# Kernel optimization log

Measured on AMD Instinct MI355X. Metric: run time of the kernel, lower is better.

## Reference

```python
import jax, jax.numpy as jnp
import numpy as np

B = 512      # batch
H = 64       # latent_dim == GRU hidden size
F = 32       # n_features
S = 2048     # seq_len
NEG_SLOPE = 0.01  # nn.LeakyReLU default


def setup_inputs() -> dict:
    key = jax.random.key(0)
    ks = jax.random.split(key, 14)

    def p(k, shape, scale=0.1):
        return jax.random.normal(k, shape, dtype=jnp.float32) * scale

    return {
        "noise": jax.random.normal(ks[0], (B, H), dtype=jnp.float32),
        # GRU forward direction (layer 0): weight_ih_l0, weight_hh_l0, biases
        "W_ih_f": p(ks[1], (3 * H, H)),
        "W_hh_f": p(ks[2], (3 * H, H)),
        "b_ih_f": p(ks[3], (3 * H,)),
        "b_hh_f": p(ks[4], (3 * H,)),
        # GRU backward direction (layer 0 reverse)
        "W_ih_b": p(ks[5], (3 * H, H)),
        "W_hh_b": p(ks[6], (3 * H, H)),
        "b_ih_b": p(ks[7], (3 * H,)),
        "b_hh_b": p(ks[8], (3 * H,)),
        # latent_linear: Linear(2H -> H)
        "W_lat": p(ks[9], (H, 2 * H)),
        "b_lat": p(ks[10], (H,)),
        # output_linear: Linear(H -> F)
        "W_out": p(ks[11], (F, H)),
        "b_out": p(ks[12], (F,)),
    }


def _leaky(x):
    return jnp.where(x >= 0, x, NEG_SLOPE * x)


def _gru_cell(x, h, W_ih, W_hh, b_ih, b_hh):
    # PyTorch GRU cell: gates ordered (r, z, n)
    gi = x @ W_ih.T + b_ih          # (B, 3H)
    gh = h @ W_hh.T + b_hh          # (B, 3H)
    i_r, i_z, i_n = jnp.split(gi, 3, axis=-1)
    h_r, h_z, h_n = jnp.split(gh, 3, axis=-1)
    r = jax.nn.sigmoid(i_r + h_r)
    z = jax.nn.sigmoid(i_z + h_z)
    n = jnp.tanh(i_n + r * h_n)
    return (1.0 - z) * n + z * h


def reference(noise, W_ih_f, W_hh_f, b_ih_f, b_hh_f,
              W_ih_b, W_hh_b, b_ih_b, b_hh_b,
              W_lat, b_lat, W_out, b_out):
    # hidden_state = noise.repeat((D*n_layers,1,1)) -> both directions start at noise
    batch = noise.shape[0]

    def step(carry, _):
        x, hf, hb = carry
        # GRU on a length-1 sequence: each direction does one cell update;
        # output timestep = concat(fwd_out, bwd_out)
        hf2 = _gru_cell(x, hf, W_ih_f, W_hh_f, b_ih_f, b_hh_f)
        hb2 = _gru_cell(x, hb, W_ih_b, W_hh_b, b_ih_b, b_hh_b)
        out = jnp.concatenate([hf2, hb2], axis=-1)        # (B, 2H)
        lat = _leaky(out @ W_lat.T + b_lat)               # (B, H)
        return (lat, hf2, hb2), lat

    x0 = jnp.zeros((batch, H), dtype=noise.dtype)
    _, ys = jax.lax.scan(step, (x0, noise, noise), None, length=S)
    seq = jnp.transpose(ys, (1, 0, 2))   # (B, S, H)
    seq = _leaky(seq)                    # second LeakyReLU as in the original
    out = jax.nn.sigmoid(seq @ W_out.T + b_out)  # (B, S, F)
    return out
```

## Files before the change

kernel.cpp:

```cpp
#include <hip/hip_runtime.h>
#include <hip/hip_bf16.h>


#define NBATCH 512
#define NH 64
#define NS 2048
#define NF 32
#define MROW 16
#define LDH 72

typedef short s16x4 __attribute__((ext_vector_type(4)));
typedef short s16x8 __attribute__((ext_vector_type(8)));
typedef float f32x4 __attribute__((ext_vector_type(4)));

#define MFMA(a, b, c) __builtin_amdgcn_mfma_f32_16x16x32_bf16((a), (b), (c), 0, 0, 0)

#define NLOG2E  (-1.4426950408889634f)
#define N2LOG2E (-2.8853900817779268f)

__device__ __forceinline__ short f2bf(float f) {
    return (short)((__float_as_uint(f) + 0x8000u) >> 16);
}

__device__ __forceinline__ f32x4 v_exp2(f32x4 a) {
    f32x4 r;
#pragma unroll
    for (int i = 0; i < 4; ++i) r[i] = __builtin_amdgcn_exp2f(a[i]);
    return r;
}

__device__ __forceinline__ f32x4 v_rcp(f32x4 a) {
    f32x4 r;
#pragma unroll
    for (int i = 0; i < 4; ++i) r[i] = __builtin_amdgcn_rcpf(a[i]);
    return r;
}

__device__ __forceinline__ f32x4 v_lk(f32x4 a) {
    f32x4 b = a * 0.01f;
    f32x4 r;
#pragma unroll
    for (int i = 0; i < 4; ++i) r[i] = fmaxf(a[i], b[i]);
    return r;
}

__device__ __forceinline__ f32x4 v_sigm(f32x4 a) {
    return v_rcp(v_exp2(a * NLOG2E) + 1.0f);
}

__device__ __forceinline__ int2 pk4bf(f32x4 v) {
    union { __hip_bfloat162 b; int i; } lo, hi;
    float2 a; a.x = v[0]; a.y = v[1];
    float2 b; b.x = v[2]; b.y = v[3];
    lo.b = __float22bfloat162_rn(a);
    hi.b = __float22bfloat162_rn(b);
    int2 r; r.x = lo.i; r.y = hi.i;
    return r;
}

__device__ __forceinline__ s16x8 bfragW(const float* __restrict__ W, int ldk,
                                        int row, int kf, int quad) {
    const float* p = W + (size_t)row * ldk + kf * 32 + quad * 8;
    s16x8 r;
#pragma unroll
    for (int i = 0; i < 8; ++i) r[i] = f2bf(p[i]);
    return r;
}

__device__ __forceinline__ f32x4 bias4(const float* __restrict__ p) {
    const float4 v = *(const float4*)p;
    f32x4 r = {v.x, v.y, v.z, v.w};
    return r;
}

__global__ __launch_bounds__(512)
__attribute__((amdgpu_waves_per_eu(2, 2)))
void grugan_kernel(const float* __restrict__ noise,
                   const float* __restrict__ Wihf, const float* __restrict__ Whhf,
                   const float* __restrict__ bihf, const float* __restrict__ bhhf,
                   const float* __restrict__ Wihb, const float* __restrict__ Whhb,
                   const float* __restrict__ bihb, const float* __restrict__ bhhb,
                   const float* __restrict__ Wlat, const float* __restrict__ blat,
                   const float* __restrict__ Wout, const float* __restrict__ bout,
                   float* __restrict__ out)
{
    __shared__ __align__(16) short Xs[2][MROW][LDH];
    __shared__ __align__(16) short X2s[2][MROW][LDH];
    __shared__ __align__(16) short Hs[2][2][MROW][LDH];

    const int tid  = threadIdx.x;
    const int wave = tid >> 6;
    const int lane = tid & 63;
    const int n    = lane & 15;
    const int quad = lane >> 4;
    const int row0 = blockIdx.x * MROW;

    const int dir  = wave >> 2;
    const int cb   = wave & 3;
    const int jrow = cb * 16 + n;
    const int jq   = cb * 16 + quad * 4;
    const float* Wih = dir ? Wihb : Wihf;
    const float* Whh = dir ? Whhb : Whhf;
    const float* bih = dir ? bihb : bihf;
    const float* bhh = dir ? bhhb : bhhf;

    s16x8 wir0 = bfragW(Wih, NH,   0 + jrow, 0, quad);
    s16x8 wir1 = bfragW(Wih, NH,   0 + jrow, 1, quad);
    s16x8 wiz0 = bfragW(Wih, NH,  64 + jrow, 0, quad);
    s16x8 wiz1 = bfragW(Wih, NH,  64 + jrow, 1, quad);
    s16x8 win0 = bfragW(Wih, NH, 128 + jrow, 0, quad);
    s16x8 win1 = bfragW(Wih, NH, 128 + jrow, 1, quad);
    s16x8 whr0 = bfragW(Whh, NH,   0 + jrow, 0, quad);
    s16x8 whr1 = bfragW(Whh, NH,   0 + jrow, 1, quad);
    s16x8 whz0 = bfragW(Whh, NH,  64 + jrow, 0, quad);
    s16x8 whz1 = bfragW(Whh, NH,  64 + jrow, 1, quad);
    s16x8 whn0 = bfragW(Whh, NH, 128 + jrow, 0, quad);
    s16x8 whn1 = bfragW(Whh, NH, 128 + jrow, 1, quad);
    f32x4 initR, initZ;
    {
        f32x4 a = bias4(&bih[jq]),      b = bias4(&bhh[jq]);
        initR = a + b;
        f32x4 c = bias4(&bih[64 + jq]), d = bias4(&bhh[64 + jq]);
        initZ = c + d;
    }
    const f32x4 initN1 = bias4(&bih[128 + jq]);
    const f32x4 initN2 = bias4(&bhh[128 + jq]);

    const int nq = (wave & 3) * 16 + quad * 4;
    s16x8 wl0 = bfragW(Wlat, 2 * NH, (wave & 3) * 16 + n, 0, quad);
    s16x8 wl1 = bfragW(Wlat, 2 * NH, (wave & 3) * 16 + n, 1, quad);
    s16x8 wl2 = bfragW(Wlat, 2 * NH, (wave & 3) * 16 + n, 2, quad);
    s16x8 wl3 = bfragW(Wlat, 2 * NH, (wave & 3) * 16 + n, 3, quad);
    const f32x4 initL = bias4(&blat[(wave & 3) * 16 + quad * 4]);

    const int f0 = (wave & 1) * 16;
    s16x8 wo0 = bfragW(Wout, NH, f0 + n, 0, quad);
    s16x8 wo1 = bfragW(Wout, NH, f0 + n, 1, quad);
    const f32x4 initO = bias4(&bout[f0 + quad * 4]);
    float* const orow = out + (size_t)(row0 + n) * (NS * NF) + f0 + quad * 4;

    for (int idx = tid; idx < MROW * LDH; idx += 512) (&Xs[0][0][0])[idx] = 0;
    f32x4 hreg;
    {
        const float4 nz = *(const float4*)&noise[(size_t)(row0 + n) * NH + jq];
        hreg[0] = nz.x; hreg[1] = nz.y; hreg[2] = nz.z; hreg[3] = nz.w;
        *(int2*)&Hs[0][dir][n][jq] = pk4bf(hreg);
    }
    __syncthreads();

    f32x4 accR, accZ, accN2;
    {
        s16x8 ha0 = *(const s16x8*)&Hs[0][dir][n][quad * 8];
        s16x8 ha1 = *(const s16x8*)&Hs[0][dir][n][32 + quad * 8];
        accR  = MFMA(whr0, ha0, initR);  accR  = MFMA(whr1, ha1, accR);
        accZ  = MFMA(whz0, ha0, initZ);  accZ  = MFMA(whz1, ha1, accZ);
        accN2 = MFMA(whn0, ha0, initN2); accN2 = MFMA(whn1, ha1, accN2);
    }

    f32x4 yv = {0.f, 0.f, 0.f, 0.f};

#define STEP(HB, T) do {                                                        \
    if ((T) >= 2 && wave >= 6)                                                  \
        *(f32x4*)(orow + (size_t)((T) - 2) * NF) = yv;                          \
    {                                                                           \
        s16x8 xa0 = *(const s16x8*)&Xs[HB][n][quad * 8];                        \
        s16x8 xa1 = *(const s16x8*)&Xs[HB][n][32 + quad * 8];                   \
        accR = MFMA(wir0, xa0, accR);   accR = MFMA(wir1, xa1, accR);           \
        accZ = MFMA(wiz0, xa0, accZ);   accZ = MFMA(wiz1, xa1, accZ);           \
        f32x4 accN1 = MFMA(win0, xa0, initN1);                                  \
        accN1 = MFMA(win1, xa1, accN1);                                         \
         \
         \
         \
        f32x4 eR = v_exp2(accR * NLOG2E);                                       \
        f32x4 rr = v_rcp(eR + 1.0f);                                            \
        f32x4 u  = accN1 + rr * accN2;                                          \
        f32x4 eU = v_exp2(u * N2LOG2E);                                         \
        f32x4 eZ = v_exp2(accZ * NLOG2E);                                       \
        f32x4 numer = (eZ + hreg) + eU * (hreg - eZ);                           \
        f32x4 denom = (eU + 1.0f) * (eZ + 1.0f);                                \
        hreg = numer * v_rcp(denom);                                            \
        *(int2*)&Hs[(HB) ^ 1][dir][n][jq] = pk4bf(hreg);                        \
    }                                                                           \
    __syncthreads();                              \
    {                                                                           \
        s16x8 ha0 = *(const s16x8*)&Hs[(HB) ^ 1][dir][n][quad * 8];             \
        s16x8 ha1 = *(const s16x8*)&Hs[(HB) ^ 1][dir][n][32 + quad * 8];        \
        if (wave < 4) {                                                         \
                                    \
            s16x8 ba0 = *(const s16x8*)&Hs[(HB) ^ 1][1][n][quad * 8];           \
            s16x8 ba1 = *(const s16x8*)&Hs[(HB) ^ 1][1][n][32 + quad * 8];      \
            f32x4 lac = MFMA(wl0, ha0, initL);                                  \
            lac = MFMA(wl1, ha1, lac);                                          \
            lac = MFMA(wl2, ba0, lac);                                          \
            lac = MFMA(wl3, ba1, lac);                                          \
            f32x4 la = v_lk(lac);                                               \
            *(int2*)&Xs[(HB) ^ 1][n][nq]  = pk4bf(la);                          \
            *(int2*)&X2s[(HB) ^ 1][n][nq] = pk4bf(v_lk(la));                    \
        } else if (wave >= 6 && (T) >= 1) {                                     \
            s16x8 p0 = *(const s16x8*)&X2s[HB][n][quad * 8];                    \
            s16x8 p1 = *(const s16x8*)&X2s[HB][n][32 + quad * 8];               \
            f32x4 po = MFMA(wo0, p0, initO);                                    \
            po = MFMA(wo1, p1, po);                                             \
            yv = v_sigm(po);                                                    \
        }                                                                       \
                    \
        accR  = MFMA(whr0, ha0, initR);  accR  = MFMA(whr1, ha1, accR);         \
        accZ  = MFMA(whz0, ha0, initZ);  accZ  = MFMA(whz1, ha1, accZ);         \
        accN2 = MFMA(whn0, ha0, initN2); accN2 = MFMA(whn1, ha1, accN2);        \
    }                                                                           \
    __syncthreads();                              \
} while (0)

    for (int t = 0; t < NS; t += 2) {
        STEP(0, t);
        STEP(1, t + 1);
    }
#undef STEP

    if (wave >= 6) {
        *(f32x4*)(orow + (size_t)(NS - 2) * NF) = yv;
        s16x8 p0 = *(const s16x8*)&X2s[0][n][quad * 8];
        s16x8 p1 = *(const s16x8*)&X2s[0][n][32 + quad * 8];
        f32x4 po = MFMA(wo0, p0, initO);
        po = MFMA(wo1, p1, po);
        *(f32x4*)(orow + (size_t)(NS - 1) * NF) = v_sigm(po);
    }
}

extern "C" void kernel_launch(void* const* d_in, const int* in_sizes, int n_in,
                              void* d_out, int out_size, void* d_ws, size_t ws_size,
                              hipStream_t stream) {
    const float* noise = (const float*)d_in[0];
    const float* Wihf  = (const float*)d_in[1];
    const float* Whhf  = (const float*)d_in[2];
    const float* bihf  = (const float*)d_in[3];
    const float* bhhf  = (const float*)d_in[4];
    const float* Wihb  = (const float*)d_in[5];
    const float* Whhb  = (const float*)d_in[6];
    const float* bihb  = (const float*)d_in[7];
    const float* bhhb  = (const float*)d_in[8];
    const float* Wlat  = (const float*)d_in[9];
    const float* blat  = (const float*)d_in[10];
    const float* Wout  = (const float*)d_in[11];
    const float* bout  = (const float*)d_in[12];

    grugan_kernel<<<dim3(NBATCH / MROW), dim3(512), 0, stream>>>(
        noise, Wihf, Whhf, bihf, bhhf, Wihb, Whhb, bihb, bhhb,
        Wlat, blat, Wout, bout, (float*)d_out);
}
```

Baseline: 1.626 ms.

## Specialize waves into GRU, latent, output and idle roles in a 1024-thread block

Doubles the block to 16 waves and gives each group a fixed role. Waves 0-7 run the GRU cell updates, waves 8-11 compute the latent linear, waves 12-13 compute the output projection and stores, and the remaining waves only take part in the barriers. Latent work no longer sits serially on the GRU waves, so it can overlap the hidden-to-hidden MFMAs between the same pair of barriers, and each wave holds fewer weight registers. In exchange, every barrier now synchronizes twice as many waves, and the waves_per_eu hint is dropped.

```diff
diff --git a/kernel.cpp b/kernel.cpp
--- a/kernel.cpp
+++ b/kernel.cpp
@@ -9,7 +9,6 @@
 #define MROW 16
 #define LDH 72
 
-typedef short s16x4 __attribute__((ext_vector_type(4)));
 typedef short s16x8 __attribute__((ext_vector_type(8)));
 typedef float f32x4 __attribute__((ext_vector_type(4)));
 
@@ -73,8 +72,7 @@
     return r;
 }
 
-__global__ __launch_bounds__(512)
-__attribute__((amdgpu_waves_per_eu(2, 2)))
+__global__ __launch_bounds__(1024)
 void grugan_kernel(const float* __restrict__ noise,
                    const float* __restrict__ Wihf, const float* __restrict__ Whhf,
                    const float* __restrict__ bihf, const float* __restrict__ bhhf,
@@ -95,83 +93,65 @@
     const int quad = lane >> 4;
     const int row0 = blockIdx.x * MROW;
 
-    const int dir  = wave >> 2;
-    const int cb   = wave & 3;
-    const int jrow = cb * 16 + n;
-    const int jq   = cb * 16 + quad * 4;
-    const float* Wih = dir ? Wihb : Wihf;
-    const float* Whh = dir ? Whhb : Whhf;
-    const float* bih = dir ? bihb : bihf;
-    const float* bhh = dir ? bhhb : bhhf;
-
-    s16x8 wir0 = bfragW(Wih, NH,   0 + jrow, 0, quad);
-    s16x8 wir1 = bfragW(Wih, NH,   0 + jrow, 1, quad);
-    s16x8 wiz0 = bfragW(Wih, NH,  64 + jrow, 0, quad);
-    s16x8 wiz1 = bfragW(Wih, NH,  64 + jrow, 1, quad);
-    s16x8 win0 = bfragW(Wih, NH, 128 + jrow, 0, quad);
-    s16x8 win1 = bfragW(Wih, NH, 128 + jrow, 1, quad);
-    s16x8 whr0 = bfragW(Whh, NH,   0 + jrow, 0, quad);
-    s16x8 whr1 = bfragW(Whh, NH,   0 + jrow, 1, quad);
-    s16x8 whz0 = bfragW(Whh, NH,  64 + jrow, 0, quad);
-    s16x8 whz1 = bfragW(Whh, NH,  64 + jrow, 1, quad);
-    s16x8 whn0 = bfragW(Whh, NH, 128 + jrow, 0, quad);
-    s16x8 whn1 = bfragW(Whh, NH, 128 + jrow, 1, quad);
-    f32x4 initR, initZ;
-    {
-        f32x4 a = bias4(&bih[jq]),      b = bias4(&bhh[jq]);
-        initR = a + b;
-        f32x4 c = bias4(&bih[64 + jq]), d = bias4(&bhh[64 + jq]);
-        initZ = c + d;
-    }
-    const f32x4 initN1 = bias4(&bih[128 + jq]);
-    const f32x4 initN2 = bias4(&bhh[128 + jq]);
-
-    const int nq = (wave & 3) * 16 + quad * 4;
-    s16x8 wl0 = bfragW(Wlat, 2 * NH, (wave & 3) * 16 + n, 0, quad);
-    s16x8 wl1 = bfragW(Wlat, 2 * NH, (wave & 3) * 16 + n, 1, quad);
-    s16x8 wl2 = bfragW(Wlat, 2 * NH, (wave & 3) * 16 + n, 2, quad);
-    s16x8 wl3 = bfragW(Wlat, 2 * NH, (wave & 3) * 16 + n, 3, quad);
-    const f32x4 initL = bias4(&blat[(wave & 3) * 16 + quad * 4]);
-
-    const int f0 = (wave & 1) * 16;
-    s16x8 wo0 = bfragW(Wout, NH, f0 + n, 0, quad);
-    s16x8 wo1 = bfragW(Wout, NH, f0 + n, 1, quad);
-    const f32x4 initO = bias4(&bout[f0 + quad * 4]);
-    float* const orow = out + (size_t)(row0 + n) * (NS * NF) + f0 + quad * 4;
-
-    for (int idx = tid; idx < MROW * LDH; idx += 512) (&Xs[0][0][0])[idx] = 0;
-    f32x4 hreg;
-    {
-        const float4 nz = *(const float4*)&noise[(size_t)(row0 + n) * NH + jq];
+    for (int idx = tid; idx < MROW * LDH; idx += 1024) (&Xs[0][0][0])[idx] = 0;
+    f32x4 hreg = {0.f, 0.f, 0.f, 0.f};
+    const int gdir = wave >> 2;
+    const int gjq  = (wave & 3) * 16 + quad * 4;
+    if (wave < 8) {
+        const float4 nz = *(const float4*)&noise[(size_t)(row0 + n) * NH + gjq];
         hreg[0] = nz.x; hreg[1] = nz.y; hreg[2] = nz.z; hreg[3] = nz.w;
-        *(int2*)&Hs[0][dir][n][jq] = pk4bf(hreg);
+        *(int2*)&Hs[0][gdir][n][gjq] = pk4bf(hreg);
     }
     __syncthreads();
 
-    f32x4 accR, accZ, accN2;
-    {
-        s16x8 ha0 = *(const s16x8*)&Hs[0][dir][n][quad * 8];
-        s16x8 ha1 = *(const s16x8*)&Hs[0][dir][n][32 + quad * 8];
-        accR  = MFMA(whr0, ha0, initR);  accR  = MFMA(whr1, ha1, accR);
-        accZ  = MFMA(whz0, ha0, initZ);  accZ  = MFMA(whz1, ha1, accZ);
-        accN2 = MFMA(whn0, ha0, initN2); accN2 = MFMA(whn1, ha1, accN2);
-    }
-
-    f32x4 yv = {0.f, 0.f, 0.f, 0.f};
-
-#define STEP(HB, T) do {                                                        \
-    if ((T) >= 2 && wave >= 6)                                                  \
-        *(f32x4*)(orow + (size_t)((T) - 2) * NF) = yv;                          \
-    {                                                                           \
+    if (wave < 8) {
+        const int dir  = gdir;
+        const int cb   = wave & 3;
+        const int jrow = cb * 16 + n;
+        const int jq   = gjq;
+        const float* Wih = dir ? Wihb : Wihf;
+        const float* Whh = dir ? Whhb : Whhf;
+        const float* bih = dir ? bihb : bihf;
+        const float* bhh = dir ? bhhb : bhhf;
+
+        s16x8 wir0 = bfragW(Wih, NH,   0 + jrow, 0, quad);
+        s16x8 wir1 = bfragW(Wih, NH,   0 + jrow, 1, quad);
+        s16x8 wiz0 = bfragW(Wih, NH,  64 + jrow, 0, quad);
+        s16x8 wiz1 = bfragW(Wih, NH,  64 + jrow, 1, quad);
+        s16x8 win0 = bfragW(Wih, NH, 128 + jrow, 0, quad);
+        s16x8 win1 = bfragW(Wih, NH, 128 + jrow, 1, quad);
+        s16x8 whr0 = bfragW(Whh, NH,   0 + jrow, 0, quad);
+        s16x8 whr1 = bfragW(Whh, NH,   0 + jrow, 1, quad);
+        s16x8 whz0 = bfragW(Whh, NH,  64 + jrow, 0, quad);
+        s16x8 whz1 = bfragW(Whh, NH,  64 + jrow, 1, quad);
+        s16x8 whn0 = bfragW(Whh, NH, 128 + jrow, 0, quad);
+        s16x8 whn1 = bfragW(Whh, NH, 128 + jrow, 1, quad);
+        f32x4 initR, initZ;
+        {
+            f32x4 a = bias4(&bih[jq]),      b = bias4(&bhh[jq]);
+            initR = a + b;
+            f32x4 c = bias4(&bih[64 + jq]), d = bias4(&bhh[64 + jq]);
+            initZ = c + d;
+        }
+        const f32x4 initN1 = bias4(&bih[128 + jq]);
+        const f32x4 initN2 = bias4(&bhh[128 + jq]);
+
+        f32x4 accR, accZ, accN2;
+        {
+            s16x8 ha0 = *(const s16x8*)&Hs[0][dir][n][quad * 8];
+            s16x8 ha1 = *(const s16x8*)&Hs[0][dir][n][32 + quad * 8];
+            accR  = MFMA(whr0, ha0, initR);  accR  = MFMA(whr1, ha1, accR);
+            accZ  = MFMA(whz0, ha0, initZ);  accZ  = MFMA(whz1, ha1, accZ);
+            accN2 = MFMA(whn0, ha0, initN2); accN2 = MFMA(whn1, ha1, accN2);
+        }
+
+#define GSTEP(HB) do {                                                          \
         s16x8 xa0 = *(const s16x8*)&Xs[HB][n][quad * 8];                        \
         s16x8 xa1 = *(const s16x8*)&Xs[HB][n][32 + quad * 8];                   \
         accR = MFMA(wir0, xa0, accR);   accR = MFMA(wir1, xa1, accR);           \
         accZ = MFMA(wiz0, xa0, accZ);   accZ = MFMA(wiz1, xa1, accZ);           \
         f32x4 accN1 = MFMA(win0, xa0, initN1);                                  \
         accN1 = MFMA(win1, xa1, accN1);                                         \
-         \
-         \
-         \
         f32x4 eR = v_exp2(accR * NLOG2E);                                       \
         f32x4 rr = v_rcp(eR + 1.0f);                                            \
         f32x4 u  = accN1 + rr * accN2;                                          \
@@ -181,50 +161,89 @@
         f32x4 denom = (eU + 1.0f) * (eZ + 1.0f);                                \
         hreg = numer * v_rcp(denom);                                            \
         *(int2*)&Hs[(HB) ^ 1][dir][n][jq] = pk4bf(hreg);                        \
-    }                                                                           \
-    __syncthreads();                              \
-    {                                                                           \
-        s16x8 ha0 = *(const s16x8*)&Hs[(HB) ^ 1][dir][n][quad * 8];             \
-        s16x8 ha1 = *(const s16x8*)&Hs[(HB) ^ 1][dir][n][32 + quad * 8];        \
-        if (wave < 4) {                                                         \
-                                    \
-            s16x8 ba0 = *(const s16x8*)&Hs[(HB) ^ 1][1][n][quad * 8];           \
-            s16x8 ba1 = *(const s16x8*)&Hs[(HB) ^ 1][1][n][32 + quad * 8];      \
-            f32x4 lac = MFMA(wl0, ha0, initL);                                  \
-            lac = MFMA(wl1, ha1, lac);                                          \
-            lac = MFMA(wl2, ba0, lac);                                          \
-            lac = MFMA(wl3, ba1, lac);                                          \
-            f32x4 la = v_lk(lac);                                               \
-            *(int2*)&Xs[(HB) ^ 1][n][nq]  = pk4bf(la);                          \
-            *(int2*)&X2s[(HB) ^ 1][n][nq] = pk4bf(v_lk(la));                    \
-        } else if (wave >= 6 && (T) >= 1) {                                     \
+        __syncthreads();                                \
+        {                                                                       \
+            s16x8 ha0 = *(const s16x8*)&Hs[(HB) ^ 1][dir][n][quad * 8];         \
+            s16x8 ha1 = *(const s16x8*)&Hs[(HB) ^ 1][dir][n][32 + quad * 8];    \
+            accR  = MFMA(whr0, ha0, initR);  accR  = MFMA(whr1, ha1, accR);     \
+            accZ  = MFMA(whz0, ha0, initZ);  accZ  = MFMA(whz1, ha1, accZ);     \
+            accN2 = MFMA(whn0, ha0, initN2); accN2 = MFMA(whn1, ha1, accN2);    \
+        }                                                                       \
+        __syncthreads();                                \
+    } while (0)
+
+        for (int t = 0; t < NS; t += 2) {
+            GSTEP(0);
+            GSTEP(1);
+        }
+#undef GSTEP
+    } else if (wave < 12) {
+        const int lt = wave & 3;
+        const int nq = lt * 16 + quad * 4;
+        s16x8 wl0 = bfragW(Wlat, 2 * NH, lt * 16 + n, 0, quad);
+        s16x8 wl1 = bfragW(Wlat, 2 * NH, lt * 16 + n, 1, quad);
+        s16x8 wl2 = bfragW(Wlat, 2 * NH, lt * 16 + n, 2, quad);
+        s16x8 wl3 = bfragW(Wlat, 2 * NH, lt * 16 + n, 3, quad);
+        const f32x4 initL = bias4(&blat[lt * 16 + quad * 4]);
+
+#define LSTEP(HB) do {                                                          \
+        __syncthreads();                                \
+        s16x8 fa0 = *(const s16x8*)&Hs[(HB) ^ 1][0][n][quad * 8];               \
+        s16x8 fa1 = *(const s16x8*)&Hs[(HB) ^ 1][0][n][32 + quad * 8];          \
+        s16x8 ba0 = *(const s16x8*)&Hs[(HB) ^ 1][1][n][quad * 8];               \
+        s16x8 ba1 = *(const s16x8*)&Hs[(HB) ^ 1][1][n][32 + quad * 8];          \
+        f32x4 lac = MFMA(wl0, fa0, initL);                                      \
+        lac = MFMA(wl1, fa1, lac);                                              \
+        lac = MFMA(wl2, ba0, lac);                                              \
+        lac = MFMA(wl3, ba1, lac);                                              \
+        f32x4 la = v_lk(lac);                                                   \
+        *(int2*)&Xs[(HB) ^ 1][n][nq]  = pk4bf(la);                              \
+        *(int2*)&X2s[(HB) ^ 1][n][nq] = pk4bf(v_lk(la));                        \
+        __syncthreads();                                \
+    } while (0)
+
+        for (int t = 0; t < NS; t += 2) {
+            LSTEP(0);
+            LSTEP(1);
+        }
+#undef LSTEP
+    } else if (wave < 14) {
+        const int f0 = (wave & 1) * 16;
+        s16x8 wo0 = bfragW(Wout, NH, f0 + n, 0, quad);
+        s16x8 wo1 = bfragW(Wout, NH, f0 + n, 1, quad);
+        const f32x4 initO = bias4(&bout[f0 + quad * 4]);
+        float* const orow = out + (size_t)(row0 + n) * (NS * NF) + f0 + quad * 4;
+        f32x4 yv = {0.f, 0.f, 0.f, 0.f};
+
+#define OSTEP(HB, T) do {                                                       \
+        if ((T) >= 2)                                                           \
+            *(f32x4*)(orow + (size_t)((T) - 2) * NF) = yv;                      \
+        __syncthreads();                                                \
+        if ((T) >= 1) {                                                         \
             s16x8 p0 = *(const s16x8*)&X2s[HB][n][quad * 8];                    \
             s16x8 p1 = *(const s16x8*)&X2s[HB][n][32 + quad * 8];               \
             f32x4 po = MFMA(wo0, p0, initO);                                    \
             po = MFMA(wo1, p1, po);                                             \
             yv = v_sigm(po);                                                    \
         }                                                                       \
-                    \
-        accR  = MFMA(whr0, ha0, initR);  accR  = MFMA(whr1, ha1, accR);         \
-        accZ  = MFMA(whz0, ha0, initZ);  accZ  = MFMA(whz1, ha1, accZ);         \
-        accN2 = MFMA(whn0, ha0, initN2); accN2 = MFMA(whn1, ha1, accN2);        \
-    }                                                                           \
-    __syncthreads();                              \
-} while (0)
-
-    for (int t = 0; t < NS; t += 2) {
-        STEP(0, t);
-        STEP(1, t + 1);
-    }
-#undef STEP
-
-    if (wave >= 6) {
+        __syncthreads();                                                \
+    } while (0)
+
+        for (int t = 0; t < NS; t += 2) {
+            OSTEP(0, t);
+            OSTEP(1, t + 1);
+        }
+#undef OSTEP
+
         *(f32x4*)(orow + (size_t)(NS - 2) * NF) = yv;
         s16x8 p0 = *(const s16x8*)&X2s[0][n][quad * 8];
         s16x8 p1 = *(const s16x8*)&X2s[0][n][32 + quad * 8];
         f32x4 po = MFMA(wo0, p0, initO);
         po = MFMA(wo1, p1, po);
         *(f32x4*)(orow + (size_t)(NS - 1) * NF) = v_sigm(po);
+    } else {
+#pragma unroll 1
+        for (int i = 0; i < 2 * NS; ++i) __syncthreads();
     }
 }
 
@@ -245,7 +264,7 @@
     const float* Wout  = (const float*)d_in[11];
     const float* bout  = (const float*)d_in[12];
 
-    grugan_kernel<<<dim3(NBATCH / MROW), dim3(512), 0, stream>>>(
+    grugan_kernel<<<dim3(NBATCH / MROW), dim3(1024), 0, stream>>>(
         noise, Wihf, Whhf, bihf, bhhf, Wihb, Whhb, bihb, bhhb,
         Wlat, blat, Wout, bout, (float*)d_out);
 }
```

After: 1.613 ms. About the same (-0.8%).

## Compute latent projection redundantly per wave to halve barriers per step

Applied to the files above, without the earlier changes.

Each wave now computes the full 64-wide latent projection itself (16 MFMAs) from both directions' hidden states and writes it to a private scratch tile. This removes the separate latent stage and its barrier, so each timestep needs one __syncthreads instead of two. The first GRU step on noise with zero input is peeled off, and the output projection is done inline by waves 0-1 instead of being deferred on waves 6-7. The cost is more redundant MFMA work, more VGPRs for the extra Wlat fragments, and more LDS scratch.

```diff
diff --git a/kernel.cpp b/kernel.cpp
--- a/kernel.cpp
+++ b/kernel.cpp
@@ -9,7 +9,6 @@
 #define MROW 16
 #define LDH 72
 
-typedef short s16x4 __attribute__((ext_vector_type(4)));
 typedef short s16x8 __attribute__((ext_vector_type(8)));
 typedef float f32x4 __attribute__((ext_vector_type(4)));
 
@@ -56,6 +55,18 @@
     hi.b = __float22bfloat162_rn(b);
     int2 r; r.x = lo.i; r.y = hi.i;
     return r;
+}
+
+__device__ __forceinline__ f32x4 gru_up(f32x4 aR, f32x4 aZ, f32x4 aN1,
+                                        f32x4 aN2, f32x4 h) {
+    f32x4 eR = v_exp2(aR * NLOG2E);
+    f32x4 rr = v_rcp(eR + 1.0f);
+    f32x4 u  = aN1 + rr * aN2;
+    f32x4 eU = v_exp2(u * N2LOG2E);
+    f32x4 eZ = v_exp2(aZ * NLOG2E);
+    f32x4 numer = (eZ + h) + eU * (h - eZ);
+    f32x4 denom = (eU + 1.0f) * (eZ + 1.0f);
+    return numer * v_rcp(denom);
 }
 
 __device__ __forceinline__ s16x8 bfragW(const float* __restrict__ W, int ldk,
@@ -84,9 +95,9 @@
                    const float* __restrict__ Wout, const float* __restrict__ bout,
                    float* __restrict__ out)
 {
-    __shared__ __align__(16) short Xs[2][MROW][LDH];
-    __shared__ __align__(16) short X2s[2][MROW][LDH];
     __shared__ __align__(16) short Hs[2][2][MROW][LDH];
+    __shared__ __align__(16) short xscr[8][MROW][LDH];
+    __shared__ __align__(16) short x2scr[2][MROW][LDH];
 
     const int tid  = threadIdx.x;
     const int wave = tid >> 6;
@@ -126,12 +137,26 @@
     const f32x4 initN1 = bias4(&bih[128 + jq]);
     const f32x4 initN2 = bias4(&bhh[128 + jq]);
 
-    const int nq = (wave & 3) * 16 + quad * 4;
-    s16x8 wl0 = bfragW(Wlat, 2 * NH, (wave & 3) * 16 + n, 0, quad);
-    s16x8 wl1 = bfragW(Wlat, 2 * NH, (wave & 3) * 16 + n, 1, quad);
-    s16x8 wl2 = bfragW(Wlat, 2 * NH, (wave & 3) * 16 + n, 2, quad);
-    s16x8 wl3 = bfragW(Wlat, 2 * NH, (wave & 3) * 16 + n, 3, quad);
-    const f32x4 initL = bias4(&blat[(wave & 3) * 16 + quad * 4]);
+    s16x8 wl00 = bfragW(Wlat, 2 * NH,  0 + n, 0, quad);
+    s16x8 wl01 = bfragW(Wlat, 2 * NH,  0 + n, 1, quad);
+    s16x8 wl02 = bfragW(Wlat, 2 * NH,  0 + n, 2, quad);
+    s16x8 wl03 = bfragW(Wlat, 2 * NH,  0 + n, 3, quad);
+    s16x8 wl10 = bfragW(Wlat, 2 * NH, 16 + n, 0, quad);
+    s16x8 wl11 = bfragW(Wlat, 2 * NH, 16 + n, 1, quad);
+    s16x8 wl12 = bfragW(Wlat, 2 * NH, 16 + n, 2, quad);
+    s16x8 wl13 = bfragW(Wlat, 2 * NH, 16 + n, 3, quad);
+    s16x8 wl20 = bfragW(Wlat, 2 * NH, 32 + n, 0, quad);
+    s16x8 wl21 = bfragW(Wlat, 2 * NH, 32 + n, 1, quad);
+    s16x8 wl22 = bfragW(Wlat, 2 * NH, 32 + n, 2, quad);
+    s16x8 wl23 = bfragW(Wlat, 2 * NH, 32 + n, 3, quad);
+    s16x8 wl30 = bfragW(Wlat, 2 * NH, 48 + n, 0, quad);
+    s16x8 wl31 = bfragW(Wlat, 2 * NH, 48 + n, 1, quad);
+    s16x8 wl32 = bfragW(Wlat, 2 * NH, 48 + n, 2, quad);
+    s16x8 wl33 = bfragW(Wlat, 2 * NH, 48 + n, 3, quad);
+    const f32x4 bL0 = bias4(&blat[ 0 + quad * 4]);
+    const f32x4 bL1 = bias4(&blat[16 + quad * 4]);
+    const f32x4 bL2 = bias4(&blat[32 + quad * 4]);
+    const f32x4 bL3 = bias4(&blat[48 + quad * 4]);
 
     const int f0 = (wave & 1) * 16;
     s16x8 wo0 = bfragW(Wout, NH, f0 + n, 0, quad);
@@ -139,93 +164,82 @@
     const f32x4 initO = bias4(&bout[f0 + quad * 4]);
     float* const orow = out + (size_t)(row0 + n) * (NS * NF) + f0 + quad * 4;
 
-    for (int idx = tid; idx < MROW * LDH; idx += 512) (&Xs[0][0][0])[idx] = 0;
+    const f32x4 Z4 = {0.f, 0.f, 0.f, 0.f};
+
     f32x4 hreg;
     {
         const float4 nz = *(const float4*)&noise[(size_t)(row0 + n) * NH + jq];
         hreg[0] = nz.x; hreg[1] = nz.y; hreg[2] = nz.z; hreg[3] = nz.w;
+        s16x8 nf0 = bfragW(noise, NH, row0 + n, 0, quad);
+        s16x8 nf1 = bfragW(noise, NH, row0 + n, 1, quad);
+        f32x4 aR  = MFMA(whr0, nf0, initR);  aR  = MFMA(whr1, nf1, aR);
+        f32x4 aZ  = MFMA(whz0, nf0, initZ);  aZ  = MFMA(whz1, nf1, aZ);
+        f32x4 aN2 = MFMA(whn0, nf0, initN2); aN2 = MFMA(whn1, nf1, aN2);
+        hreg = gru_up(aR, aZ, initN1, aN2, hreg);
         *(int2*)&Hs[0][dir][n][jq] = pk4bf(hreg);
     }
     __syncthreads();
 
-    f32x4 accR, accZ, accN2;
-    {
-        s16x8 ha0 = *(const s16x8*)&Hs[0][dir][n][quad * 8];
-        s16x8 ha1 = *(const s16x8*)&Hs[0][dir][n][32 + quad * 8];
-        accR  = MFMA(whr0, ha0, initR);  accR  = MFMA(whr1, ha1, accR);
-        accZ  = MFMA(whz0, ha0, initZ);  accZ  = MFMA(whz1, ha1, accZ);
-        accN2 = MFMA(whn0, ha0, initN2); accN2 = MFMA(whn1, ha1, accN2);
+#define WINDOW(HB, T) do {                                                      \
+                                                   \
+    s16x8 fa0 = *(const s16x8*)&Hs[HB][0][n][quad * 8];                         \
+    s16x8 fa1 = *(const s16x8*)&Hs[HB][0][n][32 + quad * 8];                    \
+    s16x8 ba0 = *(const s16x8*)&Hs[HB][1][n][quad * 8];                         \
+    s16x8 ba1 = *(const s16x8*)&Hs[HB][1][n][32 + quad * 8];                    \
+               \
+    f32x4 c1, c2, la0, la1, la2, la3;                                           \
+    c1 = MFMA(wl00, fa0, bL0); c1 = MFMA(wl01, fa1, c1);                        \
+    c2 = MFMA(wl02, ba0, Z4);  c2 = MFMA(wl03, ba1, c2);                        \
+    la0 = v_lk(c1 + c2);                                                        \
+    c1 = MFMA(wl10, fa0, bL1); c1 = MFMA(wl11, fa1, c1);                        \
+    c2 = MFMA(wl12, ba0, Z4);  c2 = MFMA(wl13, ba1, c2);                        \
+    la1 = v_lk(c1 + c2);                                                        \
+    c1 = MFMA(wl20, fa0, bL2); c1 = MFMA(wl21, fa1, c1);                        \
+    c2 = MFMA(wl22, ba0, Z4);  c2 = MFMA(wl23, ba1, c2);                        \
+    la2 = v_lk(c1 + c2);                                                        \
+    c1 = MFMA(wl30, fa0, bL3); c1 = MFMA(wl31, fa1, c1);                        \
+    c2 = MFMA(wl32, ba0, Z4);  c2 = MFMA(wl33, ba1, c2);                        \
+    la3 = v_lk(c1 + c2);                                                        \
+               \
+    *(int2*)&xscr[wave][n][ 0 + quad * 4] = pk4bf(la0);                         \
+    *(int2*)&xscr[wave][n][16 + quad * 4] = pk4bf(la1);                         \
+    *(int2*)&xscr[wave][n][32 + quad * 4] = pk4bf(la2);                         \
+    *(int2*)&xscr[wave][n][48 + quad * 4] = pk4bf(la3);                         \
+    if (wave < 2) {                                                             \
+        *(int2*)&x2scr[wave][n][ 0 + quad * 4] = pk4bf(v_lk(la0));              \
+        *(int2*)&x2scr[wave][n][16 + quad * 4] = pk4bf(v_lk(la1));              \
+        *(int2*)&x2scr[wave][n][32 + quad * 4] = pk4bf(v_lk(la2));              \
+        *(int2*)&x2scr[wave][n][48 + quad * 4] = pk4bf(v_lk(la3));              \
+    }                                                                           \
+    s16x8 xa0 = *(const s16x8*)&xscr[wave][n][quad * 8];                        \
+    s16x8 xa1 = *(const s16x8*)&xscr[wave][n][32 + quad * 8];                   \
+                      \
+    if (wave < 2) {                                                             \
+        s16x8 p0 = *(const s16x8*)&x2scr[wave][n][quad * 8];                    \
+        s16x8 p1 = *(const s16x8*)&x2scr[wave][n][32 + quad * 8];               \
+        f32x4 po = MFMA(wo0, p0, initO);                                        \
+        po = MFMA(wo1, p1, po);                                                 \
+        *(f32x4*)(orow + (size_t)(T) * NF) = v_sigm(po);                        \
+    }                                                                           \
+                                         \
+    s16x8 ha0 = dir ? ba0 : fa0;                                                \
+    s16x8 ha1 = dir ? ba1 : fa1;                                                \
+    f32x4 gR = MFMA(wir0, xa0, initR);  gR = MFMA(wir1, xa1, gR);               \
+    f32x4 hR = MFMA(whr0, ha0, Z4);     hR = MFMA(whr1, ha1, hR);               \
+    f32x4 gZ = MFMA(wiz0, xa0, initZ);  gZ = MFMA(wiz1, xa1, gZ);               \
+    f32x4 hZ = MFMA(whz0, ha0, Z4);     hZ = MFMA(whz1, ha1, hZ);               \
+    f32x4 aN1 = MFMA(win0, xa0, initN1); aN1 = MFMA(win1, xa1, aN1);            \
+    f32x4 aN2 = MFMA(whn0, ha0, initN2); aN2 = MFMA(whn1, ha1, aN2);            \
+    hreg = gru_up(gR + hR, gZ + hZ, aN1, aN2, hreg);                            \
+    *(int2*)&Hs[(HB) ^ 1][dir][n][jq] = pk4bf(hreg);                            \
+    __syncthreads();                                                            \
+} while (0)
+
+    for (int t = 0; t < NS; t += 2) {
+        WINDOW(0, t);
+        WINDOW(1, t + 1);
     }
-
-    f32x4 yv = {0.f, 0.f, 0.f, 0.f};
-
-#define STEP(HB, T) do {                                                        \
-    if ((T) >= 2 && wave >= 6)                                                  \
-        *(f32x4*)(orow + (size_t)((T) - 2) * NF) = yv;                          \
-    {                                                                           \
-        s16x8 xa0 = *(const s16x8*)&Xs[HB][n][quad * 8];                        \
-        s16x8 xa1 = *(const s16x8*)&Xs[HB][n][32 + quad * 8];                   \
-        accR = MFMA(wir0, xa0, accR);   accR = MFMA(wir1, xa1, accR);           \
-        accZ = MFMA(wiz0, xa0, accZ);   accZ = MFMA(wiz1, xa1, accZ);           \
-        f32x4 accN1 = MFMA(win0, xa0, initN1);                                  \
-        accN1 = MFMA(win1, xa1, accN1);                                         \
-         \
-         \
-         \
-        f32x4 eR = v_exp2(accR * NLOG2E);                                       \
-        f32x4 rr = v_rcp(eR + 1.0f);                                            \
-        f32x4 u  = accN1 + rr * accN2;                                          \
-        f32x4 eU = v_exp2(u * N2LOG2E);                                         \
-        f32x4 eZ = v_exp2(accZ * NLOG2E);                                       \
-        f32x4 numer = (eZ + hreg) + eU * (hreg - eZ);                           \
-        f32x4 denom = (eU + 1.0f) * (eZ + 1.0f);                                \
-        hreg = numer * v_rcp(denom);                                            \
-        *(int2*)&Hs[(HB) ^ 1][dir][n][jq] = pk4bf(hreg);                        \
-    }                                                                           \
-    __syncthreads();                              \
-    {                                                                           \
-        s16x8 ha0 = *(const s16x8*)&Hs[(HB) ^ 1][dir][n][quad * 8];             \
-        s16x8 ha1 = *(const s16x8*)&Hs[(HB) ^ 1][dir][n][32 + quad * 8];        \
-        if (wave < 4) {                                                         \
-                                    \
-            s16x8 ba0 = *(const s16x8*)&Hs[(HB) ^ 1][1][n][quad * 8];           \
-            s16x8 ba1 = *(const s16x8*)&Hs[(HB) ^ 1][1][n][32 + quad * 8];      \
-            f32x4 lac = MFMA(wl0, ha0, initL);                                  \
-            lac = MFMA(wl1, ha1, lac);                                          \
-            lac = MFMA(wl2, ba0, lac);                                          \
-            lac = MFMA(wl3, ba1, lac);                                          \
-            f32x4 la = v_lk(lac);                                               \
-            *(int2*)&Xs[(HB) ^ 1][n][nq]  = pk4bf(la);                          \
-            *(int2*)&X2s[(HB) ^ 1][n][nq] = pk4bf(v_lk(la));                    \
-        } else if (wave >= 6 && (T) >= 1) {                                     \
-            s16x8 p0 = *(const s16x8*)&X2s[HB][n][quad * 8];                    \
-            s16x8 p1 = *(const s16x8*)&X2s[HB][n][32 + quad * 8];               \
-            f32x4 po = MFMA(wo0, p0, initO);                                    \
-            po = MFMA(wo1, p1, po);                                             \
-            yv = v_sigm(po);                                                    \
-        }                                                                       \
-                    \
-        accR  = MFMA(whr0, ha0, initR);  accR  = MFMA(whr1, ha1, accR);         \
-        accZ  = MFMA(whz0, ha0, initZ);  accZ  = MFMA(whz1, ha1, accZ);         \
-        accN2 = MFMA(whn0, ha0, initN2); accN2 = MFMA(whn1, ha1, accN2);        \
-    }                                                                           \
-    __syncthreads();                              \
-} while (0)
-
-    for (int t = 0; t < NS; t += 2) {
-        STEP(0, t);
-        STEP(1, t + 1);
-    }
-#undef STEP
-
-    if (wave >= 6) {
-        *(f32x4*)(orow + (size_t)(NS - 2) * NF) = yv;
-        s16x8 p0 = *(const s16x8*)&X2s[0][n][quad * 8];
-        s16x8 p1 = *(const s16x8*)&X2s[0][n][32 + quad * 8];
-        f32x4 po = MFMA(wo0, p0, initO);
-        po = MFMA(wo1, p1, po);
-        *(f32x4*)(orow + (size_t)(NS - 1) * NF) = v_sigm(po);
-    }
+#undef WINDOW
 }
 
 extern "C" void kernel_launch(void* const* d_in, const int* in_sizes, int n_in,
```

After: 2.508 ms. 54.2% more time.

## Pack two independent batch tiles per 1024-thread block with lighter LDS barriers

Applied to the files above, without the earlier changes.

Each block now handles two 16-row batch tiles with 16 waves, halving the grid to 16 blocks and interleaving two independent recurrences so one tile's MFMA and transcendental latency can hide behind the other's. __syncthreads is replaced by an inline-asm lgkmcnt wait plus s_barrier. Weight fragments are pinned in registers through empty asm constraints and loaded only by the waves that use them. The tradeoffs are a higher register-pressure target (4 waves per EU), fewer CUs in use, and barriers that now span twice as many waves.

```diff
diff --git a/kernel.cpp b/kernel.cpp
--- a/kernel.cpp
+++ b/kernel.cpp
@@ -9,7 +9,6 @@
 #define MROW 16
 #define LDH 72
 
-typedef short s16x4 __attribute__((ext_vector_type(4)));
 typedef short s16x8 __attribute__((ext_vector_type(8)));
 typedef float f32x4 __attribute__((ext_vector_type(4)));
 
@@ -17,6 +16,12 @@
 
 #define NLOG2E  (-1.4426950408889634f)
 #define N2LOG2E (-2.8853900817779268f)
+
+#define PIN(x) __asm__("" : "+v"(x))
+
+__device__ __forceinline__ void bar_lds() {
+    __asm__ volatile("s_waitcnt lgkmcnt(0)\n\ts_barrier" ::: "memory");
+}
 
 __device__ __forceinline__ short f2bf(float f) {
     return (short)((__float_as_uint(f) + 0x8000u) >> 16);
@@ -73,8 +78,8 @@
     return r;
 }
 
-__global__ __launch_bounds__(512)
-__attribute__((amdgpu_waves_per_eu(2, 2)))
+__global__ __launch_bounds__(1024)
+__attribute__((amdgpu_waves_per_eu(4, 4)))
 void grugan_kernel(const float* __restrict__ noise,
                    const float* __restrict__ Wihf, const float* __restrict__ Whhf,
                    const float* __restrict__ bihf, const float* __restrict__ bhhf,
@@ -84,19 +89,25 @@
                    const float* __restrict__ Wout, const float* __restrict__ bout,
                    float* __restrict__ out)
 {
-    __shared__ __align__(16) short Xs[2][MROW][LDH];
-    __shared__ __align__(16) short X2s[2][MROW][LDH];
-    __shared__ __align__(16) short Hs[2][2][MROW][LDH];
+    __shared__ __align__(16) short Xs[2][2][MROW][LDH];
+    __shared__ __align__(16) short X2s[2][2][MROW][LDH];
+    __shared__ __align__(16) short Hs[2][2][2][MROW][LDH];
 
     const int tid  = threadIdx.x;
     const int wave = tid >> 6;
     const int lane = tid & 63;
     const int n    = lane & 15;
     const int quad = lane >> 4;
-    const int row0 = blockIdx.x * MROW;
-
-    const int dir  = wave >> 2;
-    const int cb   = wave & 3;
+    const int tile = wave >> 3;
+    const int tw   = wave & 7;
+    const int row0 = blockIdx.x * (2 * MROW) + tile * MROW;
+
+    short (* const Xst)[MROW][LDH]  = Xs[tile];
+    short (* const X2st)[MROW][LDH] = X2s[tile];
+    short (* const Hst)[2][MROW][LDH] = Hs[tile];
+
+    const int dir  = tw >> 2;
+    const int cb   = tw & 3;
     const int jrow = cb * 16 + n;
     const int jq   = cb * 16 + quad * 4;
     const float* Wih = dir ? Wihb : Wihf;
@@ -123,35 +134,49 @@
         f32x4 c = bias4(&bih[64 + jq]), d = bias4(&bhh[64 + jq]);
         initZ = c + d;
     }
-    const f32x4 initN1 = bias4(&bih[128 + jq]);
-    const f32x4 initN2 = bias4(&bhh[128 + jq]);
-
-    const int nq = (wave & 3) * 16 + quad * 4;
-    s16x8 wl0 = bfragW(Wlat, 2 * NH, (wave & 3) * 16 + n, 0, quad);
-    s16x8 wl1 = bfragW(Wlat, 2 * NH, (wave & 3) * 16 + n, 1, quad);
-    s16x8 wl2 = bfragW(Wlat, 2 * NH, (wave & 3) * 16 + n, 2, quad);
-    s16x8 wl3 = bfragW(Wlat, 2 * NH, (wave & 3) * 16 + n, 3, quad);
-    const f32x4 initL = bias4(&blat[(wave & 3) * 16 + quad * 4]);
-
-    const int f0 = (wave & 1) * 16;
-    s16x8 wo0 = bfragW(Wout, NH, f0 + n, 0, quad);
-    s16x8 wo1 = bfragW(Wout, NH, f0 + n, 1, quad);
-    const f32x4 initO = bias4(&bout[f0 + quad * 4]);
+    f32x4 initN1 = bias4(&bih[128 + jq]);
+    f32x4 initN2 = bias4(&bhh[128 + jq]);
+    PIN(wir0); PIN(wir1); PIN(wiz0); PIN(wiz1); PIN(win0); PIN(win1);
+    PIN(whr0); PIN(whr1); PIN(whz0); PIN(whz1); PIN(whn0); PIN(whn1);
+    PIN(initR); PIN(initZ); PIN(initN1); PIN(initN2);
+
+    const int nq = (tw & 3) * 16 + quad * 4;
+    s16x8 wl0 = {}, wl1 = {}, wl2 = {}, wl3 = {};
+    f32x4 initL = {0.f, 0.f, 0.f, 0.f};
+    if (tw < 4) {
+        wl0 = bfragW(Wlat, 2 * NH, (tw & 3) * 16 + n, 0, quad);
+        wl1 = bfragW(Wlat, 2 * NH, (tw & 3) * 16 + n, 1, quad);
+        wl2 = bfragW(Wlat, 2 * NH, (tw & 3) * 16 + n, 2, quad);
+        wl3 = bfragW(Wlat, 2 * NH, (tw & 3) * 16 + n, 3, quad);
+        initL = bias4(&blat[(tw & 3) * 16 + quad * 4]);
+        PIN(wl0); PIN(wl1); PIN(wl2); PIN(wl3); PIN(initL);
+    }
+
+    const int f0 = (tw & 1) * 16;
+    s16x8 wo0 = {}, wo1 = {};
+    f32x4 initO = {0.f, 0.f, 0.f, 0.f};
+    if (tw >= 6) {
+        wo0 = bfragW(Wout, NH, f0 + n, 0, quad);
+        wo1 = bfragW(Wout, NH, f0 + n, 1, quad);
+        initO = bias4(&bout[f0 + quad * 4]);
+        PIN(wo0); PIN(wo1); PIN(initO);
+    }
     float* const orow = out + (size_t)(row0 + n) * (NS * NF) + f0 + quad * 4;
 
-    for (int idx = tid; idx < MROW * LDH; idx += 512) (&Xs[0][0][0])[idx] = 0;
+    for (int idx = tid; idx < 2 * 2 * MROW * LDH; idx += 1024)
+        (&Xs[0][0][0][0])[idx] = 0;
     f32x4 hreg;
     {
         const float4 nz = *(const float4*)&noise[(size_t)(row0 + n) * NH + jq];
         hreg[0] = nz.x; hreg[1] = nz.y; hreg[2] = nz.z; hreg[3] = nz.w;
-        *(int2*)&Hs[0][dir][n][jq] = pk4bf(hreg);
+        *(int2*)&Hst[0][dir][n][jq] = pk4bf(hreg);
     }
     __syncthreads();
 
     f32x4 accR, accZ, accN2;
     {
-        s16x8 ha0 = *(const s16x8*)&Hs[0][dir][n][quad * 8];
-        s16x8 ha1 = *(const s16x8*)&Hs[0][dir][n][32 + quad * 8];
+        s16x8 ha0 = *(const s16x8*)&Hst[0][dir][n][quad * 8];
+        s16x8 ha1 = *(const s16x8*)&Hst[0][dir][n][32 + quad * 8];
         accR  = MFMA(whr0, ha0, initR);  accR  = MFMA(whr1, ha1, accR);
         accZ  = MFMA(whz0, ha0, initZ);  accZ  = MFMA(whz1, ha1, accZ);
         accN2 = MFMA(whn0, ha0, initN2); accN2 = MFMA(whn1, ha1, accN2);
@@ -160,18 +185,15 @@
     f32x4 yv = {0.f, 0.f, 0.f, 0.f};
 
 #define STEP(HB, T) do {                                                        \
-    if ((T) >= 2 && wave >= 6)                                                  \
+    if ((T) >= 2 && tw >= 6)                                                    \
         *(f32x4*)(orow + (size_t)((T) - 2) * NF) = yv;                          \
     {                                                                           \
-        s16x8 xa0 = *(const s16x8*)&Xs[HB][n][quad * 8];                        \
-        s16x8 xa1 = *(const s16x8*)&Xs[HB][n][32 + quad * 8];                   \
+        s16x8 xa0 = *(const s16x8*)&Xst[HB][n][quad * 8];                       \
+        s16x8 xa1 = *(const s16x8*)&Xst[HB][n][32 + quad * 8];                  \
         accR = MFMA(wir0, xa0, accR);   accR = MFMA(wir1, xa1, accR);           \
         accZ = MFMA(wiz0, xa0, accZ);   accZ = MFMA(wiz1, xa1, accZ);           \
         f32x4 accN1 = MFMA(win0, xa0, initN1);                                  \
         accN1 = MFMA(win1, xa1, accN1);                                         \
-         \
-         \
-         \
         f32x4 eR = v_exp2(accR * NLOG2E);                                       \
         f32x4 rr = v_rcp(eR + 1.0f);                                            \
         f32x4 u  = accN1 + rr * accN2;                                          \
@@ -180,36 +202,35 @@
         f32x4 numer = (eZ + hreg) + eU * (hreg - eZ);                           \
         f32x4 denom = (eU + 1.0f) * (eZ + 1.0f);                                \
         hreg = numer * v_rcp(denom);                                            \
-        *(int2*)&Hs[(HB) ^ 1][dir][n][jq] = pk4bf(hreg);                        \
+        *(int2*)&Hst[(HB) ^ 1][dir][n][jq] = pk4bf(hreg);                       \
     }                                                                           \
-    __syncthreads();                              \
+    bar_lds();                                          \
     {                                                                           \
-        s16x8 ha0 = *(const s16x8*)&Hs[(HB) ^ 1][dir][n][quad * 8];             \
-        s16x8 ha1 = *(const s16x8*)&Hs[(HB) ^ 1][dir][n][32 + quad * 8];        \
-        if (wave < 4) {                                                         \
-                                    \
-            s16x8 ba0 = *(const s16x8*)&Hs[(HB) ^ 1][1][n][quad * 8];           \
-            s16x8 ba1 = *(const s16x8*)&Hs[(HB) ^ 1][1][n][32 + quad * 8];      \
-            f32x4 lac = MFMA(wl0, ha0, initL);                                  \
-            lac = MFMA(wl1, ha1, lac);                                          \
-            lac = MFMA(wl2, ba0, lac);                                          \
-            lac = MFMA(wl3, ba1, lac);                                          \
-            f32x4 la = v_lk(lac);                                               \
-            *(int2*)&Xs[(HB) ^ 1][n][nq]  = pk4bf(la);                          \
-            *(int2*)&X2s[(HB) ^ 1][n][nq] = pk4bf(v_lk(la));                    \
-        } else if (wave >= 6 && (T) >= 1) {                                     \
-            s16x8 p0 = *(const s16x8*)&X2s[HB][n][quad * 8];                    \
-            s16x8 p1 = *(const s16x8*)&X2s[HB][n][32 + quad * 8];               \
+        s16x8 ha0 = *(const s16x8*)&Hst[(HB) ^ 1][dir][n][quad * 8];            \
+        s16x8 ha1 = *(const s16x8*)&Hst[(HB) ^ 1][dir][n][32 + quad * 8];       \
+        if (tw < 4) {                                                           \
+                                      \
+            s16x8 ba0 = *(const s16x8*)&Hst[(HB) ^ 1][1][n][quad * 8];          \
+            s16x8 ba1 = *(const s16x8*)&Hst[(HB) ^ 1][1][n][32 + quad * 8];     \
+            f32x4 c1 = MFMA(wl0, ha0, initL);                                   \
+            c1 = MFMA(wl1, ha1, c1);                                            \
+            f32x4 c2 = MFMA(wl2, ba0, c1);                                      \
+            c2 = MFMA(wl3, ba1, c2);                                            \
+            f32x4 la = v_lk(c2);                                                \
+            *(int2*)&Xst[(HB) ^ 1][n][nq]  = pk4bf(la);                         \
+            *(int2*)&X2st[(HB) ^ 1][n][nq] = pk4bf(v_lk(la));                   \
+        } else if (tw >= 6 && (T) >= 1) {                                       \
+            s16x8 p0 = *(const s16x8*)&X2st[HB][n][quad * 8];                   \
+            s16x8 p1 = *(const s16x8*)&X2st[HB][n][32 + quad * 8];              \
             f32x4 po = MFMA(wo0, p0, initO);                                    \
             po = MFMA(wo1, p1, po);                                             \
             yv = v_sigm(po);                                                    \
         }                                                                       \
-                    \
         accR  = MFMA(whr0, ha0, initR);  accR  = MFMA(whr1, ha1, accR);         \
         accZ  = MFMA(whz0, ha0, initZ);  accZ  = MFMA(whz1, ha1, accZ);         \
         accN2 = MFMA(whn0, ha0, initN2); accN2 = MFMA(whn1, ha1, accN2);        \
     }                                                                           \
-    __syncthreads();                              \
+    bar_lds();                                          \
 } while (0)
 
     for (int t = 0; t < NS; t += 2) {
@@ -218,10 +239,10 @@
     }
 #undef STEP
 
-    if (wave >= 6) {
+    if (tw >= 6) {
         *(f32x4*)(orow + (size_t)(NS - 2) * NF) = yv;
-        s16x8 p0 = *(const s16x8*)&X2s[0][n][quad * 8];
-        s16x8 p1 = *(const s16x8*)&X2s[0][n][32 + quad * 8];
+        s16x8 p0 = *(const s16x8*)&X2st[0][n][quad * 8];
+        s16x8 p1 = *(const s16x8*)&X2st[0][n][32 + quad * 8];
         f32x4 po = MFMA(wo0, p0, initO);
         po = MFMA(wo1, p1, po);
         *(f32x4*)(orow + (size_t)(NS - 1) * NF) = v_sigm(po);
@@ -245,7 +266,7 @@
     const float* Wout  = (const float*)d_in[11];
     const float* bout  = (const float*)d_in[12];
 
-    grugan_kernel<<<dim3(NBATCH / MROW), dim3(512), 0, stream>>>(
+    grugan_kernel<<<dim3(NBATCH / (2 * MROW)), dim3(1024), 0, stream>>>(
         noise, Wihf, Whhf, bihf, bhhf, Wihb, Whhb, bihb, bhhb,
         Wlat, blat, Wout, bout, (float*)d_out);
 }
```

Measured after the change: 2.686 ms. 65.2% more time.
